# Kernel tuning notes

Measured on AMD Instinct MI355X. Metric: run time of the kernel, lower is better.

## Reference

```python
import jax, jax.numpy as jnp
import numpy as np

B, N, K, F, O = 8, 65536, 9, 32, 64


def setup_inputs() -> dict:
    key = jax.random.key(0)
    k1, k2, k3, k4, k5 = jax.random.split(key, 5)
    x = jax.random.normal(k1, (B, N, F), dtype=jnp.float32)
    neighbor_index = jax.random.randint(k2, (B, N, K), 0, N)
    t_vertex = jax.random.randint(k3, (N,), 0, N)  # unused in forward, kept for signature fidelity
    v = jnp.ones((N, 8), dtype=jnp.float32) / 8.0
    adjweight = jnp.broadcast_to(jnp.eye(K, dtype=jnp.float32)[None], (8, K, K))
    W = jax.random.normal(k4, (O, K * F), dtype=jnp.float32) * 0.02
    b = jnp.zeros((O,), dtype=jnp.float32)
    return {"x": x, "t_vertex": t_vertex, "neighbor_index": neighbor_index,
            "v": v, "adjweight": adjweight, "W": W, "b": b}


def reference(x, t_vertex, neighbor_index, v, adjweight, W, b):
    bsize, num_pts, feats = x.shape
    num_neighbor = neighbor_index.shape[-1]
    # gather neighbor features per batch: [B, N, K, F]
    x_neighbors = jax.vmap(lambda xb, ib: xb[ib])(x, neighbor_index)
    # per-point learned adjacency: [N, K, K]
    adjw = jnp.einsum('ns,skt->nkt', v, adjweight)
    # apply adjacency: [B, N, K, F] (t replaces k)
    xn = jnp.einsum('bnkf,nkt->bntf', x_neighbors, adjw)
    xn = jax.nn.elu(xn.reshape(bsize, num_pts, num_neighbor * feats))
    out = jax.nn.elu(jnp.einsum('bnd,od->bno', xn, W) + b)
    # zero out last (padding) vertex
    mask = jnp.ones((1, num_pts, 1), dtype=out.dtype).at[0, -1, 0].set(0.0)
    return out * mask
```

## Files before the change

### kernel.cpp

```cpp
#include <hip/hip_runtime.h>
#include <hip/hip_bf16.h>

#define NLOG 16
#define NN 65536
#define KK 9
#define FF 32
#define OO 64
#define DD 288
#define WSTR 296
#define CHUNK 128
#define THREADS 512
#define GRID 1024
#define PTHREADS 256
#define NBLOCKS 1024
#define TOTALP (8 * NN)
#define NCHUNKS (TOTALP / CHUNK)
#define RA_STRIDE 72
#define RB_STRIDE 10
#define NB_STRIDE 10
#define AJW 88

#define XB (TOTALP * FF / 8 / PTHREADS)
#define AB (NN * KK / PTHREADS)
#define NB (TOTALP / PTHREADS)
#define WB (OO * DD / PTHREADS)

typedef float f32x4 __attribute__((ext_vector_type(4)));
typedef float f32x2 __attribute__((ext_vector_type(2)));
typedef unsigned int u32x4 __attribute__((ext_vector_type(4)));
typedef short s16x8 __attribute__((ext_vector_type(8)));
typedef short s16x4 __attribute__((ext_vector_type(4)));

static __device__ __forceinline__ short f2bf(float f) {
    union { __hip_bfloat16 h; short s; } u;
    u.h = __float2bfloat16(f);
    return u.s;
}

static __device__ __forceinline__ void bf2f2(unsigned int p, float& lo, float& hi) {
    union { unsigned int u; float f; } a, b;
    a.u = p << 16;
    b.u = p & 0xFFFF0000u;
    lo = a.f; hi = b.f;
}
static __device__ __forceinline__ float bf1(unsigned short s) {
    union { unsigned int u; float f; } a;
    a.u = ((unsigned int)s) << 16;
    return a.f;
}

static __device__ __forceinline__ float elu1(float x) {
    return fmaxf(x, __expf(fminf(x, 0.f)) - 1.f);
}

__global__ __launch_bounds__(PTHREADS) void precvt(
    const float* __restrict__ x, unsigned short* __restrict__ xbf,
    const float* __restrict__ v, const float* __restrict__ aw,
    unsigned short* __restrict__ recA, unsigned short* __restrict__ recB,
    const int* __restrict__ nbr, unsigned short* __restrict__ nb16,
    const float* __restrict__ W, unsigned short* __restrict__ wbf)
{
    const int bid = blockIdx.x;
    if (bid < XB) {
        const size_t i = ((size_t)bid * PTHREADS + threadIdx.x) * 8;
        const f32x4 a = *(const f32x4*)(x + i);
        const f32x4 b = *(const f32x4*)(x + i + 4);
        s16x8 p;
        p[0] = f2bf(a.x); p[1] = f2bf(a.y); p[2] = f2bf(a.z); p[3] = f2bf(a.w);
        p[4] = f2bf(b.x); p[5] = f2bf(b.y); p[6] = f2bf(b.z); p[7] = f2bf(b.w);
        *(s16x8*)(xbf + i) = p;
    } else if (bid < XB + AB) {
        const int e = (bid - XB) * PTHREADS + threadIdx.x;
        const int n = e / KK;
        const int t = e - n * KK;
        const float* vr = v + n * 8;
        short o[8];
        float s8 = 0.f;
        #pragma unroll
        for (int k = 0; k < KK; ++k) {
            float s = 0.f;
            #pragma unroll
            for (int si = 0; si < 8; ++si)
                s += vr[si] * aw[si * 81 + k * 9 + t];
            if (k < 8) o[k] = f2bf(s); else s8 = s;
        }
        *(s16x8*)(recA + (size_t)n * RA_STRIDE + t * 8) = *(s16x8*)o;
        recB[(size_t)n * RB_STRIDE + t] = (unsigned short)f2bf(s8);
        if (t == 0) recB[(size_t)n * RB_STRIDE + 9] = 0;
    } else if (bid < XB + AB + NB) {
        const int p = (bid - XB - AB) * PTHREADS + threadIdx.x;
        const int* s = nbr + (size_t)p * KK;
        int r[KK];
        #pragma unroll
        for (int k = 0; k < KK; ++k) r[k] = s[k];
        unsigned int* d = (unsigned int*)(nb16 + (size_t)p * NB_STRIDE);
        #pragma unroll
        for (int j = 0; j < 4; ++j)
            d[j] = ((unsigned)r[2*j] & 0xFFFFu) | ((unsigned)r[2*j+1] << 16);
        d[4] = (unsigned)r[8] & 0xFFFFu;
    } else {
        const int i = (bid - XB - AB - NB) * PTHREADS + threadIdx.x;
        const int j     = i & 7;
        const int lane  = (i >> 3) & 63;
        const int tl    = i >> 9;
        const int t     = tl >> 2;
        const int ot    = tl & 3;
        const int o     = ot * 16 + (lane & 15);
        const int d     = t * FF + (lane >> 4) * 8 + j;
        wbf[i] = (unsigned short)f2bf(W[o * DD + d]);
    }
}

__global__ __launch_bounds__(THREADS, 2) void paiconv_main(
    const unsigned short* __restrict__ xbf,
    const unsigned short* __restrict__ nb16,
    const unsigned short* __restrict__ recA,
    const unsigned short* __restrict__ recB,
    const unsigned short* __restrict__ wbf,
    const float* __restrict__ bias,
    float* __restrict__ out)
{
    __shared__ short Wl[OO * DD];
    __shared__ unsigned short AJ[CHUNK * AJW];

    const int tid  = threadIdx.x;
    const int lane = tid & 63;
    const int wid  = tid >> 6;
    const int l15  = lane & 15;
    const int fg   = lane >> 4;
    const int fo   = fg * 8;
    const int pl   = wid * 16 + l15;

    for (int e = tid; e < OO * DD / 8; e += THREADS) {
        const u32x4 r = *(const u32x4*)(wbf + (size_t)e * 8);
        *(u32x4*)(&Wl[e * 8]) = r;
    }
    {
        const int vbase = (blockIdx.x * CHUNK) & (NN - 1);
        for (int e = tid; e < CHUNK * KK; e += THREADS) {
            const int p = e / KK;
            const int t = e - p * KK;
            const u32x4 r = *(const u32x4*)(recA + (size_t)(vbase + p) * RA_STRIDE + t * 8);
            *(u32x4*)(&AJ[p * AJW + t * 8]) = r;
        }
        if (tid < CHUNK) {
            #pragma unroll
            for (int t = 0; t < KK; ++t)
                AJ[tid * AJW + RA_STRIDE + t] =
                    recB[(size_t)(vbase + tid) * RB_STRIDE + t];
        }
    }
    __syncthreads();

    const unsigned short* ajp = &AJ[pl * AJW];
    const short* wl = &Wl[lane * 8];

    for (int ci = blockIdx.x; ci < NCHUNKS; ci += GRID) {
        const size_t P = (size_t)ci * CHUNK + pl;
        const int b = (int)(P >> NLOG);

        const unsigned int* np = (const unsigned int*)(nb16 + P * NB_STRIDE);
        const unsigned int nw0 = np[0], nw1 = np[1], nw2 = np[2], nw3 = np[3], nw4 = np[4];
        int rows[KK];
        rows[0] = nw0 & 0xFFFF; rows[1] = nw0 >> 16;
        rows[2] = nw1 & 0xFFFF; rows[3] = nw1 >> 16;
        rows[4] = nw2 & 0xFFFF; rows[5] = nw2 >> 16;
        rows[6] = nw3 & 0xFFFF; rows[7] = nw3 >> 16;
        rows[8] = nw4 & 0xFFFF;

        const unsigned short* xb = xbf + (((size_t)b) << NLOG) * FF + fo;
        f32x2 G2[KK][4];
        #pragma unroll
        for (int k = 0; k < KK; ++k) {
            const u32x4 g = *(const u32x4*)(xb + (size_t)rows[k] * FF);
            float l0,h0,l1,h1,l2,h2,l3,h3;
            bf2f2(g.x, l0, h0);
            bf2f2(g.y, l1, h1);
            bf2f2(g.z, l2, h2);
            bf2f2(g.w, l3, h3);
            G2[k][0] = f32x2{l0, h0};
            G2[k][1] = f32x2{l1, h1};
            G2[k][2] = f32x2{l2, h2};
            G2[k][3] = f32x2{l3, h3};
        }

        f32x4 acc0 = {0,0,0,0}, acc1 = {0,0,0,0}, acc2 = {0,0,0,0}, acc3 = {0,0,0,0};

        #pragma unroll 1
        for (int t = 0; t < KK; ++t) {
            float a[KK];
            {
                const u32x4 qv = *(const u32x4*)(ajp + t * 8);
                bf2f2(qv.x, a[0], a[1]);
                bf2f2(qv.y, a[2], a[3]);
                bf2f2(qv.z, a[4], a[5]);
                bf2f2(qv.w, a[6], a[7]);
                a[8] = bf1(ajp[RA_STRIDE + t]);
            }

            f32x2 xn2[4] = {{0,0},{0,0},{0,0},{0,0}};
            #pragma unroll
            for (int k = 0; k < KK; ++k) {
                const f32x2 ak = {a[k], a[k]};
                #pragma unroll
                for (int i = 0; i < 4; ++i) xn2[i] += G2[k][i] * ak;
            }
            s16x8 af;
            #pragma unroll
            for (int i = 0; i < 4; ++i) {
                af[2*i]   = f2bf(elu1(xn2[i].x));
                af[2*i+1] = f2bf(elu1(xn2[i].y));
            }

            const s16x8 b0 = *(const s16x8*)(wl + (t * 4 + 0) * 512);
            const s16x8 b1 = *(const s16x8*)(wl + (t * 4 + 1) * 512);
            const s16x8 b2 = *(const s16x8*)(wl + (t * 4 + 2) * 512);
            const s16x8 b3 = *(const s16x8*)(wl + (t * 4 + 3) * 512);
            acc0 = __builtin_amdgcn_mfma_f32_16x16x32_bf16(b0, af, acc0, 0, 0, 0);
            acc1 = __builtin_amdgcn_mfma_f32_16x16x32_bf16(b1, af, acc1, 0, 0, 0);
            acc2 = __builtin_amdgcn_mfma_f32_16x16x32_bf16(b2, af, acc2, 0, 0, 0);
            acc3 = __builtin_amdgcn_mfma_f32_16x16x32_bf16(b3, af, acc3, 0, 0, 0);
        }

        const bool zero_pt = ((P & (NN - 1)) == (NN - 1));
        float* orow = out + P * OO + fg * 4;
        #pragma unroll
        for (int ot = 0; ot < 4; ++ot) {
            const f32x4 a = (ot == 0) ? acc0 : (ot == 1) ? acc1 : (ot == 2) ? acc2 : acc3;
            const f32x4 bv = *(const f32x4*)(bias + ot * 16 + fg * 4);
            f32x4 r;
            #pragma unroll
            for (int j = 0; j < 4; ++j)
                r[j] = zero_pt ? 0.f : elu1(a[j] + bv[j]);
            *(f32x4*)(orow + ot * 16) = r;
        }
    }
}

__global__ __launch_bounds__(PTHREADS, 2) void paiconv_fb(
    const float* __restrict__ x,
    const int* __restrict__ nbr,
    const float* __restrict__ v,
    const float* __restrict__ aw,
    const float* __restrict__ W,
    const float* __restrict__ bias,
    float* __restrict__ out)
{
    __shared__ short Wl[OO * WSTR];
    __shared__ float BL[OO];
    const int tid = threadIdx.x;
    for (int e = tid; e < OO * DD / 4; e += PTHREADS) {
        int o = e / 72;
        int d4 = (e - o * 72) * 4;
        const f32x4 wv = *(const f32x4*)(W + o * DD + d4);
        s16x4 p;
        p.x = f2bf(wv.x); p.y = f2bf(wv.y); p.z = f2bf(wv.z); p.w = f2bf(wv.w);
        *(s16x4*)(&Wl[o * WSTR + d4]) = p;
    }
    if (tid < OO) BL[tid] = bias[tid];
    __syncthreads();

    const int lane = tid & 63;
    const int wid  = tid >> 6;
    const int l15  = lane & 15;
    const int fg   = lane >> 4;
    const int fo   = fg * 8;
    const int pl   = wid * 16 + l15;

    for (int ci = blockIdx.x; ci < TOTALP / 64; ci += NBLOCKS) {
        const int cbase = ci * 64;
        const int P = cbase + pl;
        const int n = P & (NN - 1);
        const int b = P >> NLOG;
        const int* nip = nbr + (size_t)P * KK;
        const float* xb = x + (((size_t)b) << NLOG) * FF;

        f32x2 G2[KK][4];
        #pragma unroll
        for (int k = 0; k < KK; ++k) {
            const float* src = xb + (size_t)nip[k] * FF + fo;
            const f32x4 g0 = *(const f32x4*)(src);
            const f32x4 g1 = *(const f32x4*)(src + 4);
            G2[k][0] = f32x2{g0.x, g0.y};
            G2[k][1] = f32x2{g0.z, g0.w};
            G2[k][2] = f32x2{g1.x, g1.y};
            G2[k][3] = f32x2{g1.z, g1.w};
        }
        float vr[8];
        #pragma unroll
        for (int si = 0; si < 8; ++si) vr[si] = v[n * 8 + si];

        f32x4 acc0 = {0,0,0,0}, acc1 = {0,0,0,0}, acc2 = {0,0,0,0}, acc3 = {0,0,0,0};
        #pragma unroll
        for (int t = 0; t < KK; ++t) {
            float a[KK];
            #pragma unroll
            for (int k = 0; k < KK; ++k) {
                float s = 0.f;
                #pragma unroll
                for (int si = 0; si < 8; ++si)
                    s += vr[si] * aw[si * 81 + k * 9 + t];
                a[k] = s;
            }
            f32x2 xn2[4] = {{0,0},{0,0},{0,0},{0,0}};
            #pragma unroll
            for (int k = 0; k < KK; ++k) {
                const f32x2 ak = {a[k], a[k]};
                #pragma unroll
                for (int i = 0; i < 4; ++i) xn2[i] += G2[k][i] * ak;
            }
            s16x8 af;
            #pragma unroll
            for (int i = 0; i < 4; ++i) {
                af[2*i]   = f2bf(elu1(xn2[i].x));
                af[2*i+1] = f2bf(elu1(xn2[i].y));
            }
            const short* wrow = &Wl[l15 * WSTR + t * FF + fo];
            s16x8 b0 = *(const s16x8*)(wrow);
            s16x8 b1 = *(const s16x8*)(wrow + 16 * WSTR);
            s16x8 b2 = *(const s16x8*)(wrow + 32 * WSTR);
            s16x8 b3 = *(const s16x8*)(wrow + 48 * WSTR);
            acc0 = __builtin_amdgcn_mfma_f32_16x16x32_bf16(b0, af, acc0, 0, 0, 0);
            acc1 = __builtin_amdgcn_mfma_f32_16x16x32_bf16(b1, af, acc1, 0, 0, 0);
            acc2 = __builtin_amdgcn_mfma_f32_16x16x32_bf16(b2, af, acc2, 0, 0, 0);
            acc3 = __builtin_amdgcn_mfma_f32_16x16x32_bf16(b3, af, acc3, 0, 0, 0);
        }
        const bool zero_pt = ((P & (NN - 1)) == (NN - 1));
        float* orow = out + (size_t)P * OO + fg * 4;
        #pragma unroll
        for (int ot = 0; ot < 4; ++ot) {
            const f32x4 a = (ot == 0) ? acc0 : (ot == 1) ? acc1 : (ot == 2) ? acc2 : acc3;
            const f32x4 bv = *(const f32x4*)&BL[ot * 16 + fg * 4];
            f32x4 r;
            #pragma unroll
            for (int j = 0; j < 4; ++j)
                r[j] = zero_pt ? 0.f : elu1(a[j] + bv[j]);
            *(f32x4*)(orow + ot * 16) = r;
        }
    }
}

extern "C" void kernel_launch(void* const* d_in, const int* in_sizes, int n_in,
                              void* d_out, int out_size, void* d_ws, size_t ws_size,
                              hipStream_t stream) {
    const float* x    = (const float*)d_in[0];
    const int*   nbr  = (const int*)d_in[2];
    const float* v    = (const float*)d_in[3];
    const float* aw   = (const float*)d_in[4];
    const float* W    = (const float*)d_in[5];
    const float* bias = (const float*)d_in[6];
    float* out = (float*)d_out;

    const size_t xbf_bytes = (size_t)TOTALP * FF * 2;
    const size_t ra_bytes  = (size_t)NN * RA_STRIDE * 2;
    const size_t rb_bytes  = (size_t)NN * RB_STRIDE * 2;
    const size_t nb_bytes  = (size_t)TOTALP * NB_STRIDE * 2;
    const size_t wb_bytes  = (size_t)OO * DD * 2;
    const size_t need = xbf_bytes + ra_bytes + rb_bytes + nb_bytes + wb_bytes;

    if (ws_size >= need) {
        char* base = (char*)d_ws;
        unsigned short* xbf  = (unsigned short*)base;  base += xbf_bytes;
        unsigned short* recA = (unsigned short*)base;  base += ra_bytes;
        unsigned short* recB = (unsigned short*)base;  base += rb_bytes;
        unsigned short* nb16 = (unsigned short*)base;  base += nb_bytes;
        unsigned short* wbf  = (unsigned short*)base;

        hipLaunchKernelGGL(precvt, dim3(XB + AB + NB + WB), dim3(PTHREADS), 0, stream,
                           x, xbf, v, aw, recA, recB, nbr, nb16, W, wbf);
        hipLaunchKernelGGL(paiconv_main, dim3(GRID), dim3(THREADS), 0, stream,
                           xbf, nb16, recA, recB, wbf, bias, out);
    } else {
        hipLaunchKernelGGL(paiconv_fb, dim3(NBLOCKS), dim3(PTHREADS), 0, stream,
                           x, nbr, v, aw, W, bias, out);
    }
}
```

Measured before the change: 148.1 us.

## Transpose adjacency record layout and reorder gather-mix loop to accumulate per neighbor

The adjacency prep now stores each row indexed by source neighbor k, holding weights for all output slots t, instead of by t. The main kernel keeps the nine gathered rows as raw bf16 vectors, converts each neighbor once, and accumulates into all nine output accumulators (xn[9][4]). The t loop with MFMAs is now fully unrolled and runs after the mixing. The aim is to avoid holding all converted fp32 neighbor features live across a serialized t loop, at the cost of 72 fp32 accumulators live and possibly higher register pressure.

After: 402.4 us. 2.72x slower.

```diff
diff --git a/kernel.cpp b/kernel.cpp
--- a/kernel.cpp
+++ b/kernel.cpp
@@ -72,21 +72,21 @@
     } else if (bid < XB + AB) {
         const int e = (bid - XB) * PTHREADS + threadIdx.x;
         const int n = e / KK;
-        const int t = e - n * KK;
+        const int k = e - n * KK;
         const float* vr = v + n * 8;
         short o[8];
         float s8 = 0.f;
         #pragma unroll
-        for (int k = 0; k < KK; ++k) {
+        for (int t = 0; t < KK; ++t) {
             float s = 0.f;
             #pragma unroll
             for (int si = 0; si < 8; ++si)
                 s += vr[si] * aw[si * 81 + k * 9 + t];
-            if (k < 8) o[k] = f2bf(s); else s8 = s;
-        }
-        *(s16x8*)(recA + (size_t)n * RA_STRIDE + t * 8) = *(s16x8*)o;
-        recB[(size_t)n * RB_STRIDE + t] = (unsigned short)f2bf(s8);
-        if (t == 0) recB[(size_t)n * RB_STRIDE + 9] = 0;
+            if (t < 8) o[t] = f2bf(s); else s8 = s;
+        }
+        *(s16x8*)(recA + (size_t)n * RA_STRIDE + k * 8) = *(s16x8*)o;
+        recB[(size_t)n * RB_STRIDE + k] = (unsigned short)f2bf(s8);
+        if (k == 0) recB[(size_t)n * RB_STRIDE + 9] = 0;
     } else if (bid < XB + AB + NB) {
         const int p = (bid - XB - AB) * PTHREADS + threadIdx.x;
         const int* s = nbr + (size_t)p * KK;
@@ -139,15 +139,15 @@
         const int vbase = (blockIdx.x * CHUNK) & (NN - 1);
         for (int e = tid; e < CHUNK * KK; e += THREADS) {
             const int p = e / KK;
-            const int t = e - p * KK;
-            const u32x4 r = *(const u32x4*)(recA + (size_t)(vbase + p) * RA_STRIDE + t * 8);
-            *(u32x4*)(&AJ[p * AJW + t * 8]) = r;
+            const int k = e - p * KK;
+            const u32x4 r = *(const u32x4*)(recA + (size_t)(vbase + p) * RA_STRIDE + k * 8);
+            *(u32x4*)(&AJ[p * AJW + k * 8]) = r;
         }
         if (tid < CHUNK) {
             #pragma unroll
-            for (int t = 0; t < KK; ++t)
-                AJ[tid * AJW + RA_STRIDE + t] =
-                    recB[(size_t)(vbase + tid) * RB_STRIDE + t];
+            for (int k = 0; k < KK; ++k)
+                AJ[tid * AJW + RA_STRIDE + k] =
+                    recB[(size_t)(vbase + tid) * RB_STRIDE + k];
         }
     }
     __syncthreads();
@@ -169,49 +169,57 @@
         rows[8] = nw4 & 0xFFFF;
 
         const unsigned short* xb = xbf + (((size_t)b) << NLOG) * FF + fo;
-        f32x2 G2[KK][4];
+        u32x4 g[KK];
+        #pragma unroll
+        for (int k = 0; k < KK; ++k)
+            g[k] = *(const u32x4*)(xb + (size_t)rows[k] * FF);
+
+        f32x2 xn[KK][4];
+        #pragma unroll
+        for (int t = 0; t < KK; ++t)
+            #pragma unroll
+            for (int i = 0; i < 4; ++i) xn[t][i] = f32x2{0.f, 0.f};
+
         #pragma unroll
         for (int k = 0; k < KK; ++k) {
-            const u32x4 g = *(const u32x4*)(xb + (size_t)rows[k] * FF);
-            float l0,h0,l1,h1,l2,h2,l3,h3;
-            bf2f2(g.x, l0, h0);
-            bf2f2(g.y, l1, h1);
-            bf2f2(g.z, l2, h2);
-            bf2f2(g.w, l3, h3);
-            G2[k][0] = f32x2{l0, h0};
-            G2[k][1] = f32x2{l1, h1};
-            G2[k][2] = f32x2{l2, h2};
-            G2[k][3] = f32x2{l3, h3};
-        }
-
-        f32x4 acc0 = {0,0,0,0}, acc1 = {0,0,0,0}, acc2 = {0,0,0,0}, acc3 = {0,0,0,0};
-
-        #pragma unroll 1
-        for (int t = 0; t < KK; ++t) {
+            f32x2 gk[4];
+            {
+                float l0,h0,l1,h1,l2,h2,l3,h3;
+                bf2f2(g[k].x, l0, h0);
+                bf2f2(g[k].y, l1, h1);
+                bf2f2(g[k].z, l2, h2);
+                bf2f2(g[k].w, l3, h3);
+                gk[0] = f32x2{l0, h0};
+                gk[1] = f32x2{l1, h1};
+                gk[2] = f32x2{l2, h2};
+                gk[3] = f32x2{l3, h3};
+            }
             float a[KK];
             {
-                const u32x4 qv = *(const u32x4*)(ajp + t * 8);
-                bf2f2(qv.x, a[0], a[1]);
-                bf2f2(qv.y, a[2], a[3]);
-                bf2f2(qv.z, a[4], a[5]);
-                bf2f2(qv.w, a[6], a[7]);
-                a[8] = bf1(ajp[RA_STRIDE + t]);
-            }
-
-            f32x2 xn2[4] = {{0,0},{0,0},{0,0},{0,0}};
-            #pragma unroll
-            for (int k = 0; k < KK; ++k) {
-                const f32x2 ak = {a[k], a[k]};
+                const u32x4 av = *(const u32x4*)(ajp + k * 8);
+                bf2f2(av.x, a[0], a[1]);
+                bf2f2(av.y, a[2], a[3]);
+                bf2f2(av.z, a[4], a[5]);
+                bf2f2(av.w, a[6], a[7]);
+                a[8] = bf1(ajp[RA_STRIDE + k]);
+            }
+            #pragma unroll
+            for (int t = 0; t < KK; ++t) {
+                const f32x2 at = {a[t], a[t]};
                 #pragma unroll
-                for (int i = 0; i < 4; ++i) xn2[i] += G2[k][i] * ak;
-            }
+                for (int i = 0; i < 4; ++i) xn[t][i] += gk[i] * at;
+            }
+        }
+
+        f32x4 acc0 = {0,0,0,0}, acc1 = {0,0,0,0}, acc2 = {0,0,0,0}, acc3 = {0,0,0,0};
+        #pragma unroll
+        for (int t = 0; t < KK; ++t) {
             s16x8 af;
             #pragma unroll
             for (int i = 0; i < 4; ++i) {
-                af[2*i]   = f2bf(elu1(xn2[i].x));
-                af[2*i+1] = f2bf(elu1(xn2[i].y));
-            }
-
+                af[2*i]   = f2bf(elu1(xn[t][i].x));
+                af[2*i+1] = f2bf(elu1(xn[t][i].y));
+            }
             const s16x8 b0 = *(const s16x8*)(wl + (t * 4 + 0) * 512);
             const s16x8 b1 = *(const s16x8*)(wl + (t * 4 + 1) * 512);
             const s16x8 b2 = *(const s16x8*)(wl + (t * 4 + 2) * 512);
```

## Software-pipeline neighbor gathers across chunk rounds with double-buffered registers

Applied to the files above, without the earlier changes.

Replaces the per-chunk loop with a fixed four-round schedule. The neighbor-index load and the bf16 feature gather for the next chunk are issued before the current chunk's adjacency/MFMA compute runs, using two register buffers. The aim is to hide global gather latency behind compute. In exchange it raises register pressure (two sets of 9 u32x4 plus row indices), which may hurt occupancy at 512 threads with launch bounds 2, and it hard-codes ROUNDS = NCHUNKS/GRID.

Result: slower. 171.0 us (+15.5%).

```diff
diff --git a/kernel.cpp b/kernel.cpp
--- a/kernel.cpp
+++ b/kernel.cpp
@@ -11,6 +11,7 @@
 #define CHUNK 128
 #define THREADS 512
 #define GRID 1024
+#define ROUNDS 4
 #define PTHREADS 256
 #define NBLOCKS 1024
 #define TOTALP (8 * NN)
@@ -111,6 +112,94 @@
     }
 }
 
+
+#define LOADNBR(rw, rr)                                                     \
+{                                                                           \
+    const size_t P_ = (size_t)(blockIdx.x + (rr) * GRID) * CHUNK + pl;      \
+    const unsigned int* np_ = (const unsigned int*)(nb16 + P_ * NB_STRIDE); \
+    const unsigned int w0 = np_[0], w1 = np_[1], w2 = np_[2];               \
+    const unsigned int w3 = np_[3], w4 = np_[4];                            \
+    rw[0] = w0 & 0xFFFF; rw[1] = w0 >> 16;                                  \
+    rw[2] = w1 & 0xFFFF; rw[3] = w1 >> 16;                                  \
+    rw[4] = w2 & 0xFFFF; rw[5] = w2 >> 16;                                  \
+    rw[6] = w3 & 0xFFFF; rw[7] = w3 >> 16;                                  \
+    rw[8] = w4 & 0xFFFF;                                                    \
+}
+
+#define GATHER(gp, rw, rr)                                                  \
+{                                                                           \
+    const size_t P_ = (size_t)(blockIdx.x + (rr) * GRID) * CHUNK + pl;      \
+    const unsigned short* xb_ = xbf + ((P_ >> NLOG) << NLOG) * FF + fo;     \
+    _Pragma("unroll")                                                       \
+    for (int k_ = 0; k_ < KK; ++k_)                                         \
+        gp[k_] = *(const u32x4*)(xb_ + (size_t)rw[k_] * FF);                \
+}
+
+#define COMPUTE(gp, rr)                                                     \
+{                                                                           \
+    const size_t P_ = (size_t)(blockIdx.x + (rr) * GRID) * CHUNK + pl;      \
+    f32x2 G2[KK][4];                                                        \
+    _Pragma("unroll")                                                       \
+    for (int k_ = 0; k_ < KK; ++k_) {                                       \
+        float l0,h0,l1,h1,l2,h2,l3,h3;                                      \
+        bf2f2(gp[k_].x, l0, h0);                                            \
+        bf2f2(gp[k_].y, l1, h1);                                            \
+        bf2f2(gp[k_].z, l2, h2);                                            \
+        bf2f2(gp[k_].w, l3, h3);                                            \
+        G2[k_][0] = f32x2{l0, h0};                                          \
+        G2[k_][1] = f32x2{l1, h1};                                          \
+        G2[k_][2] = f32x2{l2, h2};                                          \
+        G2[k_][3] = f32x2{l3, h3};                                          \
+    }                                                                       \
+    f32x4 acc0 = {0,0,0,0}, acc1 = {0,0,0,0};                               \
+    f32x4 acc2 = {0,0,0,0}, acc3 = {0,0,0,0};                               \
+    _Pragma("unroll 1")                                                     \
+    for (int t_ = 0; t_ < KK; ++t_) {                                       \
+        float a_[KK];                                                       \
+        {                                                                   \
+            const u32x4 qv_ = *(const u32x4*)(ajp + t_ * 8);                \
+            bf2f2(qv_.x, a_[0], a_[1]);                                     \
+            bf2f2(qv_.y, a_[2], a_[3]);                                     \
+            bf2f2(qv_.z, a_[4], a_[5]);                                     \
+            bf2f2(qv_.w, a_[6], a_[7]);                                     \
+            a_[8] = bf1(ajp[RA_STRIDE + t_]);                               \
+        }                                                                   \
+        f32x2 xn2_[4] = {{0,0},{0,0},{0,0},{0,0}};                          \
+        _Pragma("unroll")                                                   \
+        for (int k_ = 0; k_ < KK; ++k_) {                                   \
+            const f32x2 ak_ = {a_[k_], a_[k_]};                             \
+            _Pragma("unroll")                                               \
+            for (int i_ = 0; i_ < 4; ++i_) xn2_[i_] += G2[k_][i_] * ak_;    \
+        }                                                                   \
+        s16x8 af_;                                                          \
+        _Pragma("unroll")                                                   \
+        for (int i_ = 0; i_ < 4; ++i_) {                                    \
+            af_[2*i_]   = f2bf(elu1(xn2_[i_].x));                           \
+            af_[2*i_+1] = f2bf(elu1(xn2_[i_].y));                           \
+        }                                                                   \
+        const s16x8 b0_ = *(const s16x8*)(wl + (t_ * 4 + 0) * 512);         \
+        const s16x8 b1_ = *(const s16x8*)(wl + (t_ * 4 + 1) * 512);         \
+        const s16x8 b2_ = *(const s16x8*)(wl + (t_ * 4 + 2) * 512);         \
+        const s16x8 b3_ = *(const s16x8*)(wl + (t_ * 4 + 3) * 512);         \
+        acc0 = __builtin_amdgcn_mfma_f32_16x16x32_bf16(b0_, af_, acc0,0,0,0);\
+        acc1 = __builtin_amdgcn_mfma_f32_16x16x32_bf16(b1_, af_, acc1,0,0,0);\
+        acc2 = __builtin_amdgcn_mfma_f32_16x16x32_bf16(b2_, af_, acc2,0,0,0);\
+        acc3 = __builtin_amdgcn_mfma_f32_16x16x32_bf16(b3_, af_, acc3,0,0,0);\
+    }                                                                       \
+    const bool zp_ = ((P_ & (NN - 1)) == (NN - 1));                         \
+    float* orow_ = out + P_ * OO + fg * 4;                                  \
+    _Pragma("unroll")                                                       \
+    for (int ot_ = 0; ot_ < 4; ++ot_) {                                     \
+        const f32x4 av_ = (ot_==0)?acc0:(ot_==1)?acc1:(ot_==2)?acc2:acc3;   \
+        const f32x4 bv_ = *(const f32x4*)(bias + ot_ * 16 + fg * 4);        \
+        f32x4 rr_;                                                          \
+        _Pragma("unroll")                                                   \
+        for (int j_ = 0; j_ < 4; ++j_)                                      \
+            rr_[j_] = zp_ ? 0.f : elu1(av_[j_] + bv_[j_]);                  \
+        *(f32x4*)(orow_ + ot_ * 16) = rr_;                                  \
+    }                                                                       \
+}
+
 __global__ __launch_bounds__(THREADS, 2) void paiconv_main(
     const unsigned short* __restrict__ xbf,
     const unsigned short* __restrict__ nb16,
@@ -155,85 +244,24 @@
     const unsigned short* ajp = &AJ[pl * AJW];
     const short* wl = &Wl[lane * 8];
 
-    for (int ci = blockIdx.x; ci < NCHUNKS; ci += GRID) {
-        const size_t P = (size_t)ci * CHUNK + pl;
-        const int b = (int)(P >> NLOG);
-
-        const unsigned int* np = (const unsigned int*)(nb16 + P * NB_STRIDE);
-        const unsigned int nw0 = np[0], nw1 = np[1], nw2 = np[2], nw3 = np[3], nw4 = np[4];
-        int rows[KK];
-        rows[0] = nw0 & 0xFFFF; rows[1] = nw0 >> 16;
-        rows[2] = nw1 & 0xFFFF; rows[3] = nw1 >> 16;
-        rows[4] = nw2 & 0xFFFF; rows[5] = nw2 >> 16;
-        rows[6] = nw3 & 0xFFFF; rows[7] = nw3 >> 16;
-        rows[8] = nw4 & 0xFFFF;
-
-        const unsigned short* xb = xbf + (((size_t)b) << NLOG) * FF + fo;
-        f32x2 G2[KK][4];
-        #pragma unroll
-        for (int k = 0; k < KK; ++k) {
-            const u32x4 g = *(const u32x4*)(xb + (size_t)rows[k] * FF);
-            float l0,h0,l1,h1,l2,h2,l3,h3;
-            bf2f2(g.x, l0, h0);
-            bf2f2(g.y, l1, h1);
-            bf2f2(g.z, l2, h2);
-            bf2f2(g.w, l3, h3);
-            G2[k][0] = f32x2{l0, h0};
-            G2[k][1] = f32x2{l1, h1};
-            G2[k][2] = f32x2{l2, h2};
-            G2[k][3] = f32x2{l3, h3};
-        }
-
-        f32x4 acc0 = {0,0,0,0}, acc1 = {0,0,0,0}, acc2 = {0,0,0,0}, acc3 = {0,0,0,0};
-
-        #pragma unroll 1
-        for (int t = 0; t < KK; ++t) {
-            float a[KK];
-            {
-                const u32x4 qv = *(const u32x4*)(ajp + t * 8);
-                bf2f2(qv.x, a[0], a[1]);
-                bf2f2(qv.y, a[2], a[3]);
-                bf2f2(qv.z, a[4], a[5]);
-                bf2f2(qv.w, a[6], a[7]);
-                a[8] = bf1(ajp[RA_STRIDE + t]);
-            }
-
-            f32x2 xn2[4] = {{0,0},{0,0},{0,0},{0,0}};
-            #pragma unroll
-            for (int k = 0; k < KK; ++k) {
-                const f32x2 ak = {a[k], a[k]};
-                #pragma unroll
-                for (int i = 0; i < 4; ++i) xn2[i] += G2[k][i] * ak;
-            }
-            s16x8 af;
-            #pragma unroll
-            for (int i = 0; i < 4; ++i) {
-                af[2*i]   = f2bf(elu1(xn2[i].x));
-                af[2*i+1] = f2bf(elu1(xn2[i].y));
-            }
-
-            const s16x8 b0 = *(const s16x8*)(wl + (t * 4 + 0) * 512);
-            const s16x8 b1 = *(const s16x8*)(wl + (t * 4 + 1) * 512);
-            const s16x8 b2 = *(const s16x8*)(wl + (t * 4 + 2) * 512);
-            const s16x8 b3 = *(const s16x8*)(wl + (t * 4 + 3) * 512);
-            acc0 = __builtin_amdgcn_mfma_f32_16x16x32_bf16(b0, af, acc0, 0, 0, 0);
-            acc1 = __builtin_amdgcn_mfma_f32_16x16x32_bf16(b1, af, acc1, 0, 0, 0);
-            acc2 = __builtin_amdgcn_mfma_f32_16x16x32_bf16(b2, af, acc2, 0, 0, 0);
-            acc3 = __builtin_amdgcn_mfma_f32_16x16x32_bf16(b3, af, acc3, 0, 0, 0);
-        }
-
-        const bool zero_pt = ((P & (NN - 1)) == (NN - 1));
-        float* orow = out + P * OO + fg * 4;
-        #pragma unroll
-        for (int ot = 0; ot < 4; ++ot) {
-            const f32x4 a = (ot == 0) ? acc0 : (ot == 1) ? acc1 : (ot == 2) ? acc2 : acc3;
-            const f32x4 bv = *(const f32x4*)(bias + ot * 16 + fg * 4);
-            f32x4 r;
-            #pragma unroll
-            for (int j = 0; j < 4; ++j)
-                r[j] = zero_pt ? 0.f : elu1(a[j] + bv[j]);
-            *(f32x4*)(orow + ot * 16) = r;
-        }
+    int rows0[KK], rows1[KK];
+    u32x4 g0[KK], g1[KK];
+
+    LOADNBR(rows0, 0);
+    GATHER(g0, rows0, 0);
+    LOADNBR(rows1, 1);
+
+    #pragma unroll 1
+    for (int rp = 0; rp < ROUNDS / 2; ++rp) {
+        const int r0 = 2 * rp, r1 = 2 * rp + 1;
+        GATHER(g1, rows1, r1);
+        if (rp < ROUNDS / 2 - 1) LOADNBR(rows0, r0 + 2);
+        COMPUTE(g0, r0);
+        if (rp < ROUNDS / 2 - 1) {
+            GATHER(g0, rows0, r0 + 2);
+            LOADNBR(rows1, r1 + 2);
+        }
+        COMPUTE(g1, r1);
     }
 }
 
```
